# Optimization experiments

Hardware: AMD Instinct MI355X
Metric: run time of the kernel (lower is better)

## Reference

```python
import jax, jax.numpy as jnp
import numpy as np

DIM = 2048
N_HEADS = 16
HEAD_DIM = DIM // N_HEADS
GROUP_SIZE = 128
THRESHOLD = 0.5
EPS = 1e-8
B, T = 2, 2048


def _ternary_dequant(w):
    # groupwise absmean ternary quantize + dequant; DIM % GROUP_SIZE == 0 so no pad
    O, I = w.shape
    g = I // GROUP_SIZE
    wg = w.reshape(O, g, GROUP_SIZE)
    scale = jnp.clip(jnp.mean(jnp.abs(wg), axis=-1, keepdims=True), EPS)
    wn = wg / scale
    q = jnp.where(wn > THRESHOLD, 1.0, jnp.where(wn < -THRESHOLD, -1.0, 0.0))
    return (q * scale).reshape(O, I)


def _bitlinear(x, w):
    # STE: forward uses quantized weight
    w_ste = w + jax.lax.stop_gradient(_ternary_dequant(w) - w)
    return x @ w_ste.T


def _rope_tables(t, head_dim, base=10000.0):
    half = head_dim // 2
    inv_freq = 1.0 / (base ** (jnp.arange(half, dtype=jnp.float32) / half))
    freqs = jnp.outer(jnp.arange(t, dtype=jnp.float32), inv_freq)  # [T, half]
    return jnp.cos(freqs), jnp.sin(freqs)


def _apply_rope(x, cos, sin):
    # x: [B, H, T, D]
    d = x.shape[-1]
    x1, x2 = x[..., : d // 2], x[..., d // 2 :]
    cos = cos[None, None, :, :]
    sin = sin[None, None, :, :]
    return jnp.concatenate([x1 * cos - x2 * sin, x1 * sin + x2 * cos], axis=-1)


def setup_inputs() -> dict:
    key = jax.random.key(0)
    ks = jax.random.split(key, 5)
    std = 1.0 / np.sqrt(DIM)
    return {
        "x": jax.random.normal(ks[0], (B, T, DIM), dtype=jnp.float32),
        "w_q": jax.random.normal(ks[1], (DIM, DIM), dtype=jnp.float32) * std,
        "w_k": jax.random.normal(ks[2], (DIM, DIM), dtype=jnp.float32) * std,
        "w_v": jax.random.normal(ks[3], (DIM, DIM), dtype=jnp.float32) * std,
        "w_o": jax.random.normal(ks[4], (DIM, DIM), dtype=jnp.float32) * std,
    }


def reference(x, w_q, w_k, w_v, w_o):
    b, t, c = x.shape
    scale = HEAD_DIM ** -0.5

    def split_heads(y):
        return y.reshape(b, t, N_HEADS, HEAD_DIM).transpose(0, 2, 1, 3)  # [B,H,T,D]

    q = split_heads(_bitlinear(x, w_q))
    k = split_heads(_bitlinear(x, w_k))
    v = split_heads(_bitlinear(x, w_v))

    cos, sin = _rope_tables(t, HEAD_DIM)
    q = _apply_rope(q, cos, sin)
    k = _apply_rope(k, cos, sin)

    scores = jnp.einsum("bhqd,bhkd->bhqk", q, k) * scale
    causal = jnp.triu(jnp.ones((t, t), dtype=bool), k=1)
    scores = jnp.where(causal[None, None], -jnp.inf, scores)
    probs = jax.nn.softmax(scores, axis=-1)
    y = jnp.einsum("bhqk,bhkd->bhqd", probs, v)
    y = y.transpose(0, 2, 1, 3).reshape(b, t, c)
    return _bitlinear(y, w_o)
```

## Files before the change

### kernel.cpp

```cpp
#include <hip/hip_runtime.h>
#include <stdint.h>
#include <math.h>

#define DIMC 2048
#define NHEADS 16
#define HDIM 128
#define TSEQ 2048
#define NTOK 4096

using bf16x8 = __attribute__((ext_vector_type(8))) short;
using f32x4  = __attribute__((ext_vector_type(4))) float;

typedef __attribute__((address_space(1))) const void gas_void;
typedef __attribute__((address_space(3))) void las_void;

static __device__ __forceinline__ unsigned short f2b(float f) {
  union { float f; unsigned int u; } a; a.f = f;
  unsigned int u = a.u;
  u = (u + 0x7fffu + ((u >> 16) & 1u)) >> 16;
  return (unsigned short)u;
}
static __device__ __forceinline__ float b2f(unsigned short s) {
  union { unsigned int u; float f; } a; a.u = ((unsigned int)s) << 16;
  return a.f;
}

static __device__ __forceinline__ int detect_inline(const void* __restrict__ x)
{
  const int lane = threadIdx.x & 63;
  const unsigned short u = ((const unsigned short*)x)[2 * lane];
  const int e = (u >> 7) & 0xFF;
  const unsigned long long m = __ballot((e >= 112) && (e <= 135));
  return (__popcll(m) >= 32) ? 1 : 0;
}

static __device__ __forceinline__ void dequant_one(
    const void* __restrict__ w, unsigned short* __restrict__ o,
    int grp, int lane, int isbf16)
{
  float a, bq;
  if (isbf16) {
    const unsigned int pk =
        ((const unsigned int*)((const unsigned short*)w + (long)grp * 128))[lane];
    a  = b2f((unsigned short)(pk & 0xffffu));
    bq = b2f((unsigned short)(pk >> 16));
  } else {
    const float2 v = ((const float2*)((const float*)w + (long)grp * 128))[lane];
    a = v.x; bq = v.y;
  }
  double s = fabs((double)a) + fabs((double)bq);
  #pragma unroll
  for (int off = 1; off < 64; off <<= 1) s += __shfl_xor(s, off);
  double scale = s * (1.0 / 128.0);
  if (scale < 1e-8) scale = 1e-8;
  const float fs = (float)scale;
  const double wn0 = (double)a / scale;
  const double wn1 = (double)bq / scale;
  const float q0 = (wn0 > 0.5) ? fs : ((wn0 < -0.5) ? -fs : 0.0f);
  const float q1 = (wn1 > 0.5) ? fs : ((wn1 < -0.5) ? -fs : 0.0f);
  const unsigned int opk = (unsigned int)f2b(q0) | ((unsigned int)f2b(q1) << 16);
  ((unsigned int*)o)[(long)grp * 64 + lane] = opk;
}

__global__ void __launch_bounds__(256) prep(
    const void* __restrict__ x,
    const void* __restrict__ w0, const void* __restrict__ w1,
    const void* __restrict__ w2, const void* __restrict__ w3,
    unsigned short* __restrict__ xb, unsigned short* __restrict__ wqkv,
    unsigned short* __restrict__ wob)
{
  const int isbf16 = detect_inline(x);
  const int wave = threadIdx.x >> 6, lane = threadIdx.x & 63;
  const int y = blockIdx.y;
  if (y == 0) {
    const int i = (blockIdx.x * 256 + threadIdx.x) * 4;
    if (isbf16) {
      *(ushort4*)(xb + i) = *(const ushort4*)((const unsigned short*)x + i);
    } else {
      const float4 v = *(const float4*)((const float*)x + i);
      ushort4 u;
      u.x = f2b(v.x); u.y = f2b(v.y); u.z = f2b(v.z); u.w = f2b(v.w);
      *(ushort4*)(xb + i) = u;
    }
  } else if (y <= 3) {
    const void* w = (y == 1) ? w0 : (y == 2) ? w1 : w2;
    dequant_one(w, wqkv + (long)(y - 1) * DIMC * DIMC,
                blockIdx.x * 4 + wave, lane, isbf16);
  } else {
    dequant_one(w3, wob, blockIdx.x * 4 + wave, lane, isbf16);
  }
}

__global__ void __launch_bounds__(256) dequant_auto(
    const void* __restrict__ w, const void* __restrict__ x,
    unsigned short* __restrict__ o)
{
  const int isbf16 = detect_inline(x);
  dequant_one(w, o, blockIdx.x * 4 + (threadIdx.x >> 6), threadIdx.x & 63,
              isbf16);
}

__device__ __forceinline__ void storeOne(float* C, long i, float v) { C[i] = v; }
__device__ __forceinline__ void storeOne(unsigned short* C, long i, float v) { C[i] = f2b(v); }

template <typename OUTT>
static __device__ __forceinline__ void gemm_tile(
    const unsigned short* __restrict__ A, const unsigned short* __restrict__ B,
    OUTT* __restrict__ C, int m0, int n0, int Nc, int K,
    unsigned short* As, unsigned short* Bs)
{
  const int tid = threadIdx.x;
  const int wave = tid >> 6;
  const int lane = tid & 63;
  const int wr = (wave >> 1) * 64, wc = (wave & 1) * 64;
  const int c16 = lane & 15, q4 = lane >> 4;

  f32x4 acc[4][4];
  #pragma unroll
  for (int i = 0; i < 4; i++)
    #pragma unroll
    for (int j = 0; j < 4; j++)
      acc[i][j] = (f32x4){0.f, 0.f, 0.f, 0.f};

  const int srow = tid >> 2;
  const int scol = (tid & 3) * 8;
  const unsigned short* ga = A + (long)(m0 + srow) * K + scol;
  const unsigned short* gb = B + (long)(n0 + srow) * K + scol;

  for (int k0 = 0; k0 < K; k0 += 64) {
    #pragma unroll
    for (int h = 0; h < 2; h++)
      #pragma unroll
      for (int i = 0; i < 2; i++) {
        __builtin_amdgcn_global_load_lds(
            (gas_void*)(ga + (long)i * 64 * K + k0 + h * 32),
            (las_void*)(As + h * 4096 + i * 2048 + wave * 512), 16, 0, 0);
        __builtin_amdgcn_global_load_lds(
            (gas_void*)(gb + (long)i * 64 * K + k0 + h * 32),
            (las_void*)(Bs + h * 4096 + i * 2048 + wave * 512), 16, 0, 0);
      }
    __syncthreads();
    #pragma unroll
    for (int kc = 0; kc < 2; kc++) {
      bf16x8 af[4], bfr[4];
      #pragma unroll
      for (int t = 0; t < 4; t++) {
        af[t]  = *(const bf16x8*)(As + kc * 4096 + (wr + t * 16 + c16) * 32 + q4 * 8);
        bfr[t] = *(const bf16x8*)(Bs + kc * 4096 + (wc + t * 16 + c16) * 32 + q4 * 8);
      }
      #pragma unroll
      for (int mt = 0; mt < 4; mt++)
        #pragma unroll
        for (int nt = 0; nt < 4; nt++)
          acc[mt][nt] = __builtin_amdgcn_mfma_f32_16x16x32_bf16(af[mt], bfr[nt], acc[mt][nt], 0, 0, 0);
    }
    __syncthreads();
  }

  #pragma unroll
  for (int mt = 0; mt < 4; mt++) {
    const int m = m0 + wr + mt * 16 + q4 * 4;
    #pragma unroll
    for (int nt = 0; nt < 4; nt++) {
      const int n = wc + nt * 16 + c16;
      #pragma unroll
      for (int r = 0; r < 4; r++)
        storeOne(C, (long)(m + r) * Nc + n, acc[mt][nt][r]);
    }
  }
}

template <typename OUTT>
__global__ void __launch_bounds__(256) gemm_bt(
    const unsigned short* __restrict__ A, const unsigned short* __restrict__ B,
    OUTT* __restrict__ C, int M, int N, int K)
{
  __shared__ unsigned short As[128 * 64];
  __shared__ unsigned short Bs[128 * 64];
  gemm_tile<OUTT>(A, B, C + blockIdx.x * 128, blockIdx.y * 128, blockIdx.x * 128,
                  N, K, As, Bs);
}

__global__ void __launch_bounds__(256) gemm_qkv(
    const unsigned short* __restrict__ A, const unsigned short* __restrict__ B,
    unsigned short* __restrict__ C0, unsigned short* __restrict__ C1,
    unsigned short* __restrict__ C2, int K)
{
  __shared__ unsigned short As[128 * 64];
  __shared__ unsigned short Bs[128 * 64];
  const int n0 = blockIdx.x * 128;
  unsigned short* Cb = (n0 < 2048) ? C0 : (n0 < 4096) ? C1 : C2;
  gemm_tile<unsigned short>(A, B, Cb + (n0 & 2047), blockIdx.y * 128, n0,
                            DIMC, K, As, Bs);
}

__global__ void __launch_bounds__(256) rope_kernel(
    unsigned short* __restrict__ Q, unsigned short* __restrict__ Kb)
{
  const int idx = blockIdx.x * 256 + threadIdx.x;
  const int d4 = (idx & 15) * 4;
  const int h = (idx >> 4) & (NHEADS - 1);
  const int row = idx >> 8;
  const int t = row & (TSEQ - 1);
  const long base = (long)row * DIMC + h * HDIM + d4;

  ushort4 q1 = *(ushort4*)(Q + base), q2 = *(ushort4*)(Q + base + 64);
  ushort4 k1 = *(ushort4*)(Kb + base), k2 = *(ushort4*)(Kb + base + 64);
  unsigned short* q1p = (unsigned short*)&q1;
  unsigned short* q2p = (unsigned short*)&q2;
  unsigned short* k1p = (unsigned short*)&k1;
  unsigned short* k2p = (unsigned short*)&k2;

  #pragma unroll
  for (int j = 0; j < 4; j++) {
    const int d = d4 + j;
    const float inv_freq = expf(-9.210340371976184f * (float)d * (1.0f / 64.0f));
    float sn, cs;
    sincosf((float)t * inv_freq, &sn, &cs);
    float x1 = b2f(q1p[j]), x2 = b2f(q2p[j]);
    q1p[j] = f2b(x1 * cs - x2 * sn);
    q2p[j] = f2b(x1 * sn + x2 * cs);
    x1 = b2f(k1p[j]); x2 = b2f(k2p[j]);
    k1p[j] = f2b(x1 * cs - x2 * sn);
    k2p[j] = f2b(x1 * sn + x2 * cs);
  }
  *(ushort4*)(Q + base) = q1;  *(ushort4*)(Q + base + 64) = q2;
  *(ushort4*)(Kb + base) = k1; *(ushort4*)(Kb + base + 64) = k2;
}

#define FA_M 16.0f
__global__ void __launch_bounds__(256) fattn(
    const unsigned short* __restrict__ Q,
    const unsigned short* __restrict__ K,
    const unsigned short* __restrict__ V,
    unsigned short* __restrict__ Y)
{
  __shared__ unsigned short SU[9216];
  __shared__ unsigned short VT[128 * 72];
  __shared__ float red[4][32];

  const int tid = threadIdx.x, wave = tid >> 6, lane = tid & 63;
  const int idx = blockIdx.x;
  const int qt = 15 - (idx >> 5);
  const int bh = idx & 31;
  const int b = bh >> 4, h = bh & 15;
  const int qbase = qt * 128;
  const int qw = wave * 32;
  const int c = lane & 15, g = lane >> 4;
  const long tokbase = (long)b * TSEQ;
  const int col0 = h * HDIM;

  bf16x8 qf[2][4];
  #pragma unroll
  for (int qq = 0; qq < 2; qq++) {
    const unsigned short* qp =
        Q + (tokbase + qbase + qw + qq * 16 + c) * DIMC + col0 + g * 8;
    #pragma unroll
    for (int kc = 0; kc < 4; kc++) qf[qq][kc] = *(const bf16x8*)(qp + kc * 32);
  }

  f32x4 od[8][2];
  #pragma unroll
  for (int dt = 0; dt < 8; dt++)
    #pragma unroll
    for (int qq = 0; qq < 2; qq++)
      od[dt][qq] = (f32x4){0.f, 0.f, 0.f, 0.f};
  float lpart[2][4];
  #pragma unroll
  for (int qq = 0; qq < 2; qq++)
    #pragma unroll
    for (int r = 0; r < 4; r++) lpart[qq][r] = 0.0f;

  const int ksr = tid >> 2, ksc = (tid & 3) * 32;
  const int vk0 = (tid & 31) * 2, vd0 = (tid >> 5) * 16;

  const float SC = 0.088388347648318447f;
  const int nkt = 2 * qt + 2;

  float4 kr0, kr1, kr2, kr3;
  bf16x8 va0, va1, vb0, vb1;
  {
    const unsigned short* src = K + (tokbase + ksr) * DIMC + col0 + ksc;
    kr0 = ((const float4*)src)[0]; kr1 = ((const float4*)src)[1];
    kr2 = ((const float4*)src)[2]; kr3 = ((const float4*)src)[3];
    const unsigned short* s0 = V + (tokbase + vk0) * DIMC + col0 + vd0;
    const unsigned short* s1 = s0 + DIMC;
    va0 = *(const bf16x8*)(s0); va1 = *(const bf16x8*)(s0 + 8);
    vb0 = *(const bf16x8*)(s1); vb1 = *(const bf16x8*)(s1 + 8);
  }

  for (int kt = 0; kt < nkt; kt++) {
    const int kb = kt * 64;
    __syncthreads();
    {
      float4* dst = (float4*)&SU[ksr * 136 + ksc];
      dst[0] = kr0; dst[1] = kr1; dst[2] = kr2; dst[3] = kr3;
    }
    {
      #pragma unroll
      for (int dd = 0; dd < 8; dd++) {
        const unsigned int p0 =
            (unsigned int)(unsigned short)va0[dd] |
            ((unsigned int)(unsigned short)vb0[dd] << 16);
        *(unsigned int*)&VT[(vd0 + dd) * 72 + vk0] = p0;
      }
      #pragma unroll
      for (int dd = 0; dd < 8; dd++) {
        const unsigned int p1 =
            (unsigned int)(unsigned short)va1[dd] |
            ((unsigned int)(unsigned short)vb1[dd] << 16);
        *(unsigned int*)&VT[(vd0 + 8 + dd) * 72 + vk0] = p1;
      }
    }
    __syncthreads();

    if (kt + 1 < nkt) {
      const int kb2 = kb + 64;
      const unsigned short* src = K + (tokbase + kb2 + ksr) * DIMC + col0 + ksc;
      kr0 = ((const float4*)src)[0]; kr1 = ((const float4*)src)[1];
      kr2 = ((const float4*)src)[2]; kr3 = ((const float4*)src)[3];
      const unsigned short* s0 = V + (tokbase + kb2 + vk0) * DIMC + col0 + vd0;
      const unsigned short* s1 = s0 + DIMC;
      va0 = *(const bf16x8*)(s0); va1 = *(const bf16x8*)(s0 + 8);
      vb0 = *(const bf16x8*)(s1); vb1 = *(const bf16x8*)(s1 + 8);
    }

    f32x4 sacc[2][4];
    #pragma unroll
    for (int qq = 0; qq < 2; qq++)
      #pragma unroll
      for (int nt = 0; nt < 4; nt++) sacc[qq][nt] = (f32x4){0.f, 0.f, 0.f, 0.f};
    #pragma unroll
    for (int kc = 0; kc < 4; kc++) {
      bf16x8 bk[4];
      #pragma unroll
      for (int nt = 0; nt < 4; nt++)
        bk[nt] = *(const bf16x8*)&SU[(nt * 16 + c) * 136 + kc * 32 + g * 8];
      #pragma unroll
      for (int qq = 0; qq < 2; qq++)
        #pragma unroll
        for (int nt = 0; nt < 4; nt++)
          sacc[qq][nt] = __builtin_amdgcn_mfma_f32_16x16x32_bf16(
              qf[qq][kc], bk[nt], sacc[qq][nt], 0, 0, 0);
    }
    __syncthreads();

    #pragma unroll
    for (int qq = 0; qq < 2; qq++)
      #pragma unroll
      for (int r = 0; r < 4; r++) {
        const int qg = qbase + qw + qq * 16 + g * 4 + r;
        #pragma unroll
        for (int nt = 0; nt < 4; nt++) {
          const int kg = kb + nt * 16 + c;
          const float sv = sacc[qq][nt][r] * SC - FA_M;
          const float p = (kg > qg) ? 0.0f : __expf(sv);
          lpart[qq][r] += p;
          SU[(wave * 32 + qq * 16 + g * 4 + r) * 72 + nt * 16 + c] = f2b(p);
        }
      }

    #pragma unroll
    for (int kc = 0; kc < 2; kc++) {
      bf16x8 pb[2];
      #pragma unroll
      for (int qq = 0; qq < 2; qq++)
        pb[qq] = *(const bf16x8*)&SU[(wave * 32 + qq * 16 + c) * 72 + kc * 32 + g * 8];
      #pragma unroll
      for (int dt = 0; dt < 8; dt++) {
        bf16x8 va = *(const bf16x8*)&VT[(dt * 16 + c) * 72 + kc * 32 + g * 8];
        #pragma unroll
        for (int qq = 0; qq < 2; qq++)
          od[dt][qq] = __builtin_amdgcn_mfma_f32_16x16x32_bf16(
              va, pb[qq], od[dt][qq], 0, 0, 0);
      }
    }
  }

  #pragma unroll
  for (int qq = 0; qq < 2; qq++)
    #pragma unroll
    for (int r = 0; r < 4; r++) {
      float l = lpart[qq][r];
      #pragma unroll
      for (int off = 1; off < 16; off <<= 1) l += __shfl_xor(l, off);
      lpart[qq][r] = l;
    }
  __syncthreads();
  if (c == 0) {
    #pragma unroll
    for (int qq = 0; qq < 2; qq++)
      #pragma unroll
      for (int r = 0; r < 4; r++)
        red[wave][qq * 16 + g * 4 + r] = 1.0f / lpart[qq][r];
  }
  __syncthreads();
  #pragma unroll
  for (int qq = 0; qq < 2; qq++) {
    const float linv = red[wave][qq * 16 + c];
    unsigned short* yp =
        Y + (tokbase + qbase + qw + qq * 16 + c) * DIMC + col0;
    #pragma unroll
    for (int dt = 0; dt < 8; dt++)
      #pragma unroll
      for (int r = 0; r < 4; r++)
        yp[dt * 16 + g * 4 + r] = f2b(od[dt][qq][r] * linv);
  }
}

extern "C" void kernel_launch(void* const* d_in, const int* in_sizes, int n_in,
                              void* d_out, int out_size, void* d_ws, size_t ws_size,
                              hipStream_t stream)
{
  const void* x  = d_in[0];
  const void* wq = d_in[1];
  const void* wk = d_in[2];
  const void* wv = d_in[3];
  const void* wo = d_in[4];
  float* out = (float*)d_out;

  char* ws = (char*)d_ws;
  const size_t MB = 1024 * 1024;
  unsigned short* wbuf = (unsigned short*)(ws + 0 * MB);
  unsigned short* xb   = (unsigned short*)(ws + 24 * MB);
  unsigned short* Qb   = (unsigned short*)(ws + 40 * MB);
  unsigned short* Kb   = (unsigned short*)(ws + 56 * MB);
  unsigned short* Vb   = (unsigned short*)(ws + 72 * MB);
  unsigned short* wob  = (unsigned short*)(ws + 88 * MB);
  unsigned short* Yb   = xb;

  const int wo_in_prep = (ws_size >= 97 * MB) ? 1 : 0;

  prep<<<dim3(8192, wo_in_prep ? 5 : 4), 256, 0, stream>>>(
      x, wq, wk, wv, wo, xb, wbuf, wob);
  gemm_qkv<<<dim3(48, 32), 256, 0, stream>>>(xb, wbuf, Qb, Kb, Vb, DIMC);
  rope_kernel<<<dim3(4096), 256, 0, stream>>>(Qb, Kb);
  fattn<<<dim3(512), 256, 0, stream>>>(Qb, Kb, Vb, Yb);
  const unsigned short* wo_b;
  if (wo_in_prep) {
    wo_b = wob;
  } else {
    dequant_auto<<<dim3(8192), 256, 0, stream>>>(wo, x, wbuf);
    wo_b = wbuf;
  }
  gemm_bt<float><<<dim3(16, 32), 256, 0, stream>>>(Yb, wo_b, out, NTOK, DIMC, DIMC);
}
```

Measured before the change: 410.4 us.

## Replace GEMM tiles with 8-wave double-buffered, swizzled 256x128 pipeline

Replaces the single-buffered 128x128 GEMM tile (4 waves, load then sync then compute) with a 512-thread, 256x128 tile that shares the B tile across two A halves. The core double-buffers LDS, issues next-tile global-to-LDS loads while MFMAs run, splits the compute into two halves around a B prefetch, uses explicit waitcnt and barriers, raises wave priority during MFMA, and XOR-swizzles the LDS layout to reduce bank conflicts. Both the QKV projection and the output projection use it. The fine-grained manual synchronisation adds complexity and risk of races. The larger LDS footprint (96KB per block) also limits occupancy.

```diff
diff --git a/kernel.cpp b/kernel.cpp
--- a/kernel.cpp
+++ b/kernel.cpp
@@ -100,98 +100,154 @@
               isbf16);
 }
 
-__device__ __forceinline__ void storeOne(float* C, long i, float v) { C[i] = v; }
-__device__ __forceinline__ void storeOne(unsigned short* C, long i, float v) { C[i] = f2b(v); }
-
-template <typename OUTT>
-static __device__ __forceinline__ void gemm_tile(
-    const unsigned short* __restrict__ A, const unsigned short* __restrict__ B,
-    OUTT* __restrict__ C, int m0, int n0, int Nc, int K,
-    unsigned short* As, unsigned short* Bs)
+static __device__ __forceinline__ void gemm8_core(
+    const unsigned short* __restrict__ A, const unsigned short* __restrict__ Bm,
+    int m0, int n0, int K, f32x4 (&acc)[4][4],
+    unsigned short (*sm)[3][8192])
 {
   const int tid = threadIdx.x;
-  const int wave = tid >> 6;
-  const int lane = tid & 63;
-  const int wr = (wave >> 1) * 64, wc = (wave & 1) * 64;
+  const int w = tid >> 6, lane = tid & 63;
+  const int wr = w >> 1, wc = w & 1;
   const int c16 = lane & 15, q4 = lane >> 4;
-
-  f32x4 acc[4][4];
+  const int swz = (c16 * 32 + q4 * 8) ^ ((c16 & 8) ? 16 : 0);
+  const int srow = lane >> 2;
+  const int scol = ((lane & 3) * 8) ^ ((lane & 32) ? 16 : 0);
+  const int rg0 = w >> 1, cg = w & 1;
+  const int NT = K >> 6;
+
   #pragma unroll
   for (int i = 0; i < 4; i++)
     #pragma unroll
-    for (int j = 0; j < 4; j++)
-      acc[i][j] = (f32x4){0.f, 0.f, 0.f, 0.f};
-
-  const int srow = tid >> 2;
-  const int scol = (tid & 3) * 8;
-  const unsigned short* ga = A + (long)(m0 + srow) * K + scol;
-  const unsigned short* gb = B + (long)(n0 + srow) * K + scol;
-
-  for (int k0 = 0; k0 < K; k0 += 64) {
-    #pragma unroll
-    for (int h = 0; h < 2; h++)
-      #pragma unroll
-      for (int i = 0; i < 2; i++) {
-        __builtin_amdgcn_global_load_lds(
-            (gas_void*)(ga + (long)i * 64 * K + k0 + h * 32),
-            (las_void*)(As + h * 4096 + i * 2048 + wave * 512), 16, 0, 0);
-        __builtin_amdgcn_global_load_lds(
-            (gas_void*)(gb + (long)i * 64 * K + k0 + h * 32),
-            (las_void*)(Bs + h * 4096 + i * 2048 + wave * 512), 16, 0, 0);
+    for (int j = 0; j < 4; j++) acc[i][j] = (f32x4){0.f, 0.f, 0.f, 0.f};
+
+  auto stage = [&](const unsigned short* __restrict__ G, int rowbase, int kt,
+                   unsigned short* dst) {
+    #pragma unroll
+    for (int l = 0; l < 2; l++) {
+      const unsigned short* s = G +
+          (long)(rowbase + (rg0 + l * 4) * 16 + srow) * K + kt * 64 + cg * 32 + scol;
+      __builtin_amdgcn_global_load_lds((gas_void*)s,
+          (las_void*)(dst + (l * 8 + w) * 512), 16, 0, 0);
+    }
+  };
+
+  stage(A,  m0,       0, sm[0][0]);
+  stage(A,  m0 + 128, 0, sm[0][1]);
+  stage(Bm, n0,       0, sm[0][2]);
+  stage(Bm, n0,       1, sm[1][2]);
+  asm volatile("s_waitcnt vmcnt(2)" ::: "memory");
+  __builtin_amdgcn_s_barrier();
+
+  bf16x8 af[4][2], b01[2][2], b23[2][2];
+  const int ah = wr >> 1;
+  const int abase = (wr & 1) * 4096;
+  const int bbase = wc * 4096;
+
+  for (int t = 0; t < NT; ++t) {
+    const int cur = t & 1, nxt = cur ^ 1;
+
+    #pragma unroll
+    for (int m = 0; m < 4; m++)
+      #pragma unroll
+      for (int kk = 0; kk < 2; kk++)
+        af[m][kk] = *(const bf16x8*)&sm[cur][ah][abase + m * 1024 + kk * 512 + swz];
+    #pragma unroll
+    for (int n = 0; n < 2; n++)
+      #pragma unroll
+      for (int kk = 0; kk < 2; kk++) {
+        b01[n][kk] = *(const bf16x8*)&sm[cur][2][bbase + n * 1024 + kk * 512 + swz];
+        b23[n][kk] = *(const bf16x8*)&sm[cur][2][bbase + (2 + n) * 1024 + kk * 512 + swz];
       }
-    __syncthreads();
-    #pragma unroll
-    for (int kc = 0; kc < 2; kc++) {
-      bf16x8 af[4], bfr[4];
-      #pragma unroll
-      for (int t = 0; t < 4; t++) {
-        af[t]  = *(const bf16x8*)(As + kc * 4096 + (wr + t * 16 + c16) * 32 + q4 * 8);
-        bfr[t] = *(const bf16x8*)(Bs + kc * 4096 + (wc + t * 16 + c16) * 32 + q4 * 8);
-      }
-      #pragma unroll
-      for (int mt = 0; mt < 4; mt++)
+    if (t + 1 < NT) {
+      stage(A, m0,       t + 1, sm[nxt][0]);
+      stage(A, m0 + 128, t + 1, sm[nxt][1]);
+    }
+    __builtin_amdgcn_s_barrier();
+    asm volatile("s_waitcnt lgkmcnt(0)" ::: "memory");
+    __builtin_amdgcn_s_setprio(1);
+    #pragma unroll
+    for (int kk = 0; kk < 2; kk++)
+      #pragma unroll
+      for (int m = 0; m < 4; m++)
         #pragma unroll
-        for (int nt = 0; nt < 4; nt++)
-          acc[mt][nt] = __builtin_amdgcn_mfma_f32_16x16x32_bf16(af[mt], bfr[nt], acc[mt][nt], 0, 0, 0);
-    }
-    __syncthreads();
-  }
-
-  #pragma unroll
-  for (int mt = 0; mt < 4; mt++) {
-    const int m = m0 + wr + mt * 16 + q4 * 4;
-    #pragma unroll
-    for (int nt = 0; nt < 4; nt++) {
-      const int n = wc + nt * 16 + c16;
-      #pragma unroll
-      for (int r = 0; r < 4; r++)
-        storeOne(C, (long)(m + r) * Nc + n, acc[mt][nt][r]);
-    }
-  }
-}
-
-template <typename OUTT>
-__global__ void __launch_bounds__(256) gemm_bt(
-    const unsigned short* __restrict__ A, const unsigned short* __restrict__ B,
-    OUTT* __restrict__ C, int M, int N, int K)
-{
-  __shared__ unsigned short As[128 * 64];
-  __shared__ unsigned short Bs[128 * 64];
-  gemm_tile<OUTT>(A, B, C + blockIdx.x * 128, blockIdx.y * 128, blockIdx.x * 128,
-                  N, K, As, Bs);
-}
-
-__global__ void __launch_bounds__(256) gemm_qkv(
-    const unsigned short* __restrict__ A, const unsigned short* __restrict__ B,
+        for (int n = 0; n < 2; n++)
+          acc[m][n] = __builtin_amdgcn_mfma_f32_16x16x32_bf16(
+              af[m][kk], b01[n][kk], acc[m][n], 0, 0, 0);
+    __builtin_amdgcn_s_setprio(0);
+    __builtin_amdgcn_s_barrier();
+
+    if (t + 2 < NT) stage(Bm, n0, t + 2, sm[cur][2]);
+    __builtin_amdgcn_s_setprio(1);
+    #pragma unroll
+    for (int kk = 0; kk < 2; kk++)
+      #pragma unroll
+      for (int m = 0; m < 4; m++)
+        #pragma unroll
+        for (int n = 0; n < 2; n++)
+          acc[m][2 + n] = __builtin_amdgcn_mfma_f32_16x16x32_bf16(
+              af[m][kk], b23[n][kk], acc[m][2 + n], 0, 0, 0);
+    __builtin_amdgcn_s_setprio(0);
+    if (t + 1 < NT) {
+      if (t + 2 < NT) { asm volatile("s_waitcnt vmcnt(2)" ::: "memory"); }
+      else            { asm volatile("s_waitcnt vmcnt(0)" ::: "memory"); }
+      __builtin_amdgcn_s_barrier();
+    }
+  }
+}
+
+__global__ void __launch_bounds__(512, 2) gemm8_qkv(
+    const unsigned short* __restrict__ A, const unsigned short* __restrict__ Bm,
     unsigned short* __restrict__ C0, unsigned short* __restrict__ C1,
     unsigned short* __restrict__ C2, int K)
 {
-  __shared__ unsigned short As[128 * 64];
-  __shared__ unsigned short Bs[128 * 64];
+  __shared__ unsigned short sm[2][3][8192];
   const int n0 = blockIdx.x * 128;
+  const int m0 = blockIdx.y * 256;
+  f32x4 acc[4][4];
+  gemm8_core(A, Bm, m0, n0, K, acc, sm);
+
   unsigned short* Cb = (n0 < 2048) ? C0 : (n0 < 4096) ? C1 : C2;
-  gemm_tile<unsigned short>(A, B, Cb + (n0 & 2047), blockIdx.y * 128, n0,
-                            DIMC, K, As, Bs);
+  const int w = threadIdx.x >> 6, lane = threadIdx.x & 63;
+  const int wr = w >> 1, wc = w & 1;
+  const int c16 = lane & 15, q4 = lane >> 4;
+  const int nloc = (n0 & 2047) + wc * 64;
+  #pragma unroll
+  for (int mt = 0; mt < 4; mt++) {
+    const int m = m0 + wr * 64 + mt * 16 + q4 * 4;
+    #pragma unroll
+    for (int nt = 0; nt < 4; nt++) {
+      const int n = nloc + nt * 16 + c16;
+      #pragma unroll
+      for (int r = 0; r < 4; r++)
+        Cb[(long)(m + r) * DIMC + n] = f2b(acc[mt][nt][r]);
+    }
+  }
+}
+
+__global__ void __launch_bounds__(512, 2) gemm8_bt(
+    const unsigned short* __restrict__ A, const unsigned short* __restrict__ Bm,
+    float* __restrict__ C, int N, int K)
+{
+  __shared__ unsigned short sm[2][3][8192];
+  const int n0 = blockIdx.x * 128;
+  const int m0 = blockIdx.y * 256;
+  f32x4 acc[4][4];
+  gemm8_core(A, Bm, m0, n0, K, acc, sm);
+
+  const int w = threadIdx.x >> 6, lane = threadIdx.x & 63;
+  const int wr = w >> 1, wc = w & 1;
+  const int c16 = lane & 15, q4 = lane >> 4;
+  #pragma unroll
+  for (int mt = 0; mt < 4; mt++) {
+    const int m = m0 + wr * 64 + mt * 16 + q4 * 4;
+    #pragma unroll
+    for (int nt = 0; nt < 4; nt++) {
+      const int n = n0 + wc * 64 + nt * 16 + c16;
+      #pragma unroll
+      for (int r = 0; r < 4; r++)
+        C[(long)(m + r) * N + n] = acc[mt][nt][r];
+    }
+  }
 }
 
 __global__ void __launch_bounds__(256) rope_kernel(
@@ -433,7 +489,7 @@
 
   prep<<<dim3(8192, wo_in_prep ? 5 : 4), 256, 0, stream>>>(
       x, wq, wk, wv, wo, xb, wbuf, wob);
-  gemm_qkv<<<dim3(48, 32), 256, 0, stream>>>(xb, wbuf, Qb, Kb, Vb, DIMC);
+  gemm8_qkv<<<dim3(48, 16), 512, 0, stream>>>(xb, wbuf, Qb, Kb, Vb, DIMC);
   rope_kernel<<<dim3(4096), 256, 0, stream>>>(Qb, Kb);
   fattn<<<dim3(512), 256, 0, stream>>>(Qb, Kb, Vb, Yb);
   const unsigned short* wo_b;
@@ -443,5 +499,5 @@
     dequant_auto<<<dim3(8192), 256, 0, stream>>>(wo, x, wbuf);
     wo_b = wbuf;
   }
-  gemm_bt<float><<<dim3(16, 32), 256, 0, stream>>>(Yb, wo_b, out, NTOK, DIMC, DIMC);
-}
+  gemm8_bt<<<dim3(16, 16), 512, 0, stream>>>(Yb, wo_b, out, DIMC, DIMC);
+}
```

After: 391.7 us. 1.05x faster.
